# Performance work log

Hardware: AMD Instinct MI355X
Metric: run time of the kernel (lower is better)

The kernel has to match this reference:

```python
import jax, jax.numpy as jnp
import numpy as np

B, N, D = 4, 2048, 256
H, DA, DL = 4, 64, 64          # heads, q/k dim per head, u/v dim per head
NUM_BUCKETS = 128
LN_EPS = 1e-5


def _layernorm(x, g, b):
    mu = jnp.mean(x, axis=-1, keepdims=True)
    var = jnp.var(x, axis=-1, keepdims=True)
    return (x - mu) * jax.lax.rsqrt(var + LN_EPS) * g + b


def setup_inputs() -> dict:
    key = jax.random.key(0)
    ks = jax.random.split(key, 8)
    x = jax.random.normal(ks[0], (B, N, D), jnp.float32)
    lengths = jax.random.randint(ks[1], (B,), 1, N + 1).astype(jnp.int64)
    timestamps = jnp.sort(
        jax.random.randint(ks[2], (B, N), 0, 10_000_000), axis=1
    ).astype(jnp.int64)
    F_uvqk = H * (2 * DL + 2 * DA)
    W_uvqk = jax.random.normal(ks[3], (D, F_uvqk), jnp.float32) * 0.02
    b_uvqk = jnp.zeros((F_uvqk,), jnp.float32)
    W_o = jax.random.normal(ks[4], (H * DL, D), jnp.float32) * 0.02
    b_o = jnp.zeros((D,), jnp.float32)
    ln_in_g = jnp.ones((D,), jnp.float32)
    ln_in_b = jnp.zeros((D,), jnp.float32)
    ln_attn_g = jnp.ones((H * DL,), jnp.float32)
    ln_attn_b = jnp.zeros((H * DL,), jnp.float32)
    w_pos = jax.random.normal(ks[5], (2 * N - 1,), jnp.float32) * 0.02
    w_ts = jax.random.normal(ks[6], (NUM_BUCKETS + 1,), jnp.float32) * 0.02
    return dict(x=x, W_uvqk=W_uvqk, b_uvqk=b_uvqk, W_o=W_o, b_o=b_o,
                ln_in_g=ln_in_g, ln_in_b=ln_in_b,
                ln_attn_g=ln_attn_g, ln_attn_b=ln_attn_b,
                w_pos=w_pos, w_ts=w_ts,
                lengths=lengths, timestamps=timestamps)


def reference(x, W_uvqk, b_uvqk, W_o, b_o, ln_in_g, ln_in_b,
              ln_attn_g, ln_attn_b, w_pos, w_ts, lengths, timestamps):
    # HSTU jagged transduction unit (padded + mask representation).
    nx = _layernorm(x, ln_in_g, ln_in_b)                       # [B,N,D]
    uvqk = jax.nn.silu(nx @ W_uvqk + b_uvqk)                   # fused projection
    u, v, q, k = jnp.split(
        uvqk, [H * DL, 2 * H * DL, 2 * H * DL + H * DA], axis=-1)
    q = q.reshape(B, N, H, DA)
    k = k.reshape(B, N, H, DA)
    v = v.reshape(B, N, H, DL)
    qk = jnp.einsum('bnhd,bmhd->bhnm', q, k)                   # [B,H,N,N]

    # relative position + bucketed relative timestamp bias -> [B,N,N]
    pos = jnp.arange(N)
    pos_bias = w_pos[pos[:, None] - pos[None, :] + (N - 1)]    # [N,N]
    diff = timestamps[:, :, None] - timestamps[:, None, :]     # [B,N,N] int
    bucket = jnp.clip(
        (jnp.log(jnp.maximum(jnp.abs(diff).astype(jnp.float32), 1.0)) / 0.301)
        .astype(jnp.int32), 0, NUM_BUCKETS)
    bias = pos_bias[None] + w_ts[bucket]                       # [B,N,N]

    # non-softmax HSTU attention: silu(scores)/N, causal + valid-key mask
    attn = jax.nn.silu(qk + bias[:, None, :, :]) * (1.0 / N)
    causal = pos[:, None] >= pos[None, :]                      # [N,N]
    valid = pos[None, :] < lengths[:, None]                    # [B,N]
    mask = causal[None, None, :, :] & valid[:, None, None, :]
    attn = jnp.where(mask, attn, 0.0)

    av = jnp.einsum('bhnm,bmhd->bnhd', attn, v).reshape(B, N, H * DL)
    out = (_layernorm(av, ln_attn_g, ln_attn_b) * u) @ W_o + b_o + x
    out = jnp.where(valid[:, :, None], out, 0.0)               # zero padded rows
    return out
```

## Files before the change

kernel.cpp:

```cpp
#include <hip/hip_runtime.h>
#include <stdint.h>

#define BB 4
#define NN 2048
#define DD 256
#define HH 4

typedef __attribute__((ext_vector_type(8))) __bf16 bf16x8;
typedef __attribute__((ext_vector_type(4))) float f32x4;
typedef __attribute__((ext_vector_type(8))) unsigned short u16x8;
typedef __attribute__((ext_vector_type(4))) unsigned short u16x4;

__device__ __forceinline__ unsigned short f2bf(float f) {
  union { float f; uint32_t u; } v; v.f = f;
  uint32_t r = v.u + 0x7fffu + ((v.u >> 16) & 1u);
  return (unsigned short)(r >> 16);
}
__device__ __forceinline__ bf16x8 ld8(const unsigned short* p) {
  return __builtin_bit_cast(bf16x8, *(const u16x8*)p);
}
__device__ __forceinline__ f32x4 mfma16(bf16x8 a, bf16x8 b, f32x4 c) {
  return __builtin_amdgcn_mfma_f32_16x16x32_bf16(a, b, c, 0, 0, 0);
}
__device__ __forceinline__ float silu_f(float x) {
  return x / (1.0f + __expf(-x));
}

__global__ __launch_bounds__(256) void k_prep_w(const float* __restrict__ Wu,
                                                const float* __restrict__ Wo,
                                                unsigned short* __restrict__ Wu_t,
                                                unsigned short* __restrict__ Wo_t) {
  __shared__ float T[64][65];
  int bi = blockIdx.x;
  const float* src; unsigned short* dst; int F, f0, d0;
  if (bi < 64) { src = Wu; dst = Wu_t; F = 1024; f0 = (bi >> 2) * 64; d0 = (bi & 3) * 64; }
  else { int j = bi - 64; src = Wo; dst = Wo_t; F = 256; f0 = (j >> 2) * 64; d0 = (j & 3) * 64; }
  int t = threadIdx.x;
  int li = t >> 4;
  int lj = (t & 15) * 4;
  #pragma unroll
  for (int it = 0; it < 4; ++it) {
    int d = li + it * 16;
    float4 v = *(const float4*)(src + (size_t)(d0 + d) * F + f0 + lj);
    T[lj + 0][d] = v.x; T[lj + 1][d] = v.y; T[lj + 2][d] = v.z; T[lj + 3][d] = v.w;
  }
  __syncthreads();
  #pragma unroll
  for (int it = 0; it < 4; ++it) {
    int f = li + it * 16;
    u16x4 o;
    o[0] = f2bf(T[f][lj + 0]); o[1] = f2bf(T[f][lj + 1]);
    o[2] = f2bf(T[f][lj + 2]); o[3] = f2bf(T[f][lj + 3]);
    *(u16x4*)(dst + (size_t)(f0 + f) * 256 + d0 + lj) = o;
  }
}

__global__ __launch_bounds__(256) void k_ln_in(const float* __restrict__ x,
                                               const float* __restrict__ g,
                                               const float* __restrict__ be,
                                               unsigned short* __restrict__ nx) {
  int wave = threadIdx.x >> 6, lane = threadIdx.x & 63;
  int row = blockIdx.x * 4 + wave;
  const float4 v = *(const float4*)(x + (size_t)row * DD + lane * 4);
  float s = v.x + v.y + v.z + v.w;
  float sq = v.x * v.x + v.y * v.y + v.z * v.z + v.w * v.w;
  #pragma unroll
  for (int o = 32; o; o >>= 1) { s += __shfl_xor(s, o); sq += __shfl_xor(sq, o); }
  float mean = s * (1.0f / DD);
  float var = sq * (1.0f / DD) - mean * mean;
  float rstd = rsqrtf(var + 1e-5f);
  const float4 gv = *(const float4*)(g + lane * 4);
  const float4 bv = *(const float4*)(be + lane * 4);
  u16x4 o4;
  o4[0] = f2bf((v.x - mean) * rstd * gv.x + bv.x);
  o4[1] = f2bf((v.y - mean) * rstd * gv.y + bv.y);
  o4[2] = f2bf((v.z - mean) * rstd * gv.z + bv.z);
  o4[3] = f2bf((v.w - mean) * rstd * gv.w + bv.w);
  *(u16x4*)(nx + (size_t)row * DD + lane * 4) = o4;
}

__global__ __launch_bounds__(256) void k_gemm_uvqk(const unsigned short* __restrict__ nx,
                                                   const unsigned short* __restrict__ Wu_t,
                                                   const float* __restrict__ b_uvqk,
                                                   float* __restrict__ u,
                                                   unsigned short* __restrict__ v_tmp,
                                                   unsigned short* __restrict__ q_t,
                                                   unsigned short* __restrict__ k_t) {
  __shared__ unsigned short As[128 * 72];
  __shared__ unsigned short Bs[128 * 72];
  int tid = threadIdx.x, lane = tid & 63, w = tid >> 6;
  int wr = w >> 1, wc = w & 1, c = lane & 15, g = lane >> 4;
  int rblk = blockIdx.x >> 3, cblk = blockIdx.x & 7;
  int R0 = rblk * 128, C0 = cblk * 128;
  f32x4 acc[4][4] = {};
  for (int ks = 0; ks < 4; ++ks) {
    __syncthreads();
    #pragma unroll
    for (int it = 0; it < 4; ++it) {
      int task = tid + it * 256, row = task >> 3, ch = task & 7;
      *(u16x8*)(As + row * 72 + ch * 8) =
          *(const u16x8*)(nx + (size_t)(R0 + row) * 256 + ks * 64 + ch * 8);
      *(u16x8*)(Bs + row * 72 + ch * 8) =
          *(const u16x8*)(Wu_t + (size_t)(C0 + row) * 256 + ks * 64 + ch * 8);
    }
    __syncthreads();
    #pragma unroll
    for (int kk = 0; kk < 2; ++kk) {
      int koff = kk * 32 + g * 8;
      bf16x8 af[4], bfr[4];
      #pragma unroll
      for (int rt = 0; rt < 4; ++rt) af[rt] = ld8(As + (wr * 64 + rt * 16 + c) * 72 + koff);
      #pragma unroll
      for (int ct = 0; ct < 4; ++ct) bfr[ct] = ld8(Bs + (wc * 64 + ct * 16 + c) * 72 + koff);
      #pragma unroll
      for (int rt = 0; rt < 4; ++rt)
        #pragma unroll
        for (int ct = 0; ct < 4; ++ct)
          acc[rt][ct] = mfma16(af[rt], bfr[ct], acc[rt][ct]);
    }
  }
  #pragma unroll
  for (int rt = 0; rt < 4; ++rt) {
    #pragma unroll
    for (int ct = 0; ct < 4; ++ct) {
      int F = C0 + wc * 64 + ct * 16 + c;
      float bb = b_uvqk[F];
      #pragma unroll
      for (int rr = 0; rr < 4; ++rr) {
        int R = R0 + wr * 64 + rt * 16 + g * 4 + rr;
        float pre = acc[rt][ct][rr] + bb;
        float sv = silu_f(pre);
        int b = R >> 11, n = R & 2047;
        if (F < 256) {
          u[(size_t)R * 256 + F] = sv;
        } else if (F < 512) {
          v_tmp[(size_t)R * 256 + (F - 256)] = f2bf(sv);
        } else if (F < 768) {
          int h = (F - 512) >> 6, d = (F - 512) & 63;
          q_t[((size_t)((b << 2) + h) * 2048 + n) * 64 + d] = f2bf(sv);
        } else {
          int h = (F - 768) >> 6, d = (F - 768) & 63;
          k_t[((size_t)((b << 2) + h) * 2048 + n) * 64 + d] = f2bf(sv);
        }
      }
    }
  }
}

__global__ __launch_bounds__(256) void k_vtrans(const unsigned short* __restrict__ v_tmp,
                                                unsigned short* __restrict__ v_t) {
  __shared__ unsigned short T[64 * 72];
  int bi = blockIdx.x;
  int nch = bi & 31, h = (bi >> 5) & 3, b = bi >> 7;
  int n0 = nch * 64;
  int tid = threadIdx.x;
  #pragma unroll
  for (int it = 0; it < 2; ++it) {
    int task = tid + it * 256;
    int i = task >> 3, ch = task & 7;
    *(u16x8*)(T + i * 72 + ch * 8) =
        *(const u16x8*)(v_tmp + ((size_t)(b * 2048 + n0 + i)) * 256 + h * 64 + ch * 8);
  }
  __syncthreads();
  #pragma unroll
  for (int it = 0; it < 2; ++it) {
    int task = tid + it * 256;
    int d = task >> 3, ch = task & 7;
    u16x8 ov;
    #pragma unroll
    for (int uu = 0; uu < 8; ++uu) ov[uu] = T[(ch * 8 + uu) * 72 + d];
    *(u16x8*)(v_t + ((size_t)((b * 4 + h) * 64 + d)) * 2048 + n0 + ch * 8) = ov;
  }
}

__global__ __launch_bounds__(256) void k_attn(const unsigned short* __restrict__ q_t,
                                              const unsigned short* __restrict__ k_t,
                                              const unsigned short* __restrict__ v_t,
                                              const int* __restrict__ ts_raw,
                                              const int* __restrict__ lens_raw,
                                              const float* __restrict__ w_pos,
                                              const float* __restrict__ w_ts,
                                              float* __restrict__ avP0,
                                              float* __restrict__ avP1) {
  __shared__ unsigned short P_s[4][16 * 72];
  int tid = threadIdx.x, lane = tid & 63, h = tid >> 6;
  int c = lane & 15, g = lane >> 4;
  int bi = blockIdx.x;
  int b, qt, chunk;
  if (bi < 512) { chunk = 0; b = bi & 3; qt = 127 - (bi >> 2); }
  else { chunk = 1; int j = bi - 512; b = j & 3; qt = 127 - (j >> 2); }
  int n0 = qt * 16;
  int stride = (lens_raw[1] == 0 && lens_raw[3] == 0) ? 2 : 1;
  int Lb = lens_raw[b * stride];
  const int* tsb = ts_raw + (size_t)b * 2048 * stride;
  const unsigned short* qp = q_t + (size_t)(b * 4 + h) * 2048 * 64;
  const unsigned short* kp = k_t + (size_t)(b * 4 + h) * 2048 * 64;
  const unsigned short* vp = v_t + (size_t)(b * 4 + h) * 64 * 2048;

  int m_end = min(n0 + 16, Lb);
  int kv_lo = chunk ? 1024 : 0;
  int kv_hi = chunk ? m_end : min(m_end, 1024);

  bf16x8 qf0 = ld8(qp + (size_t)(n0 + c) * 64 + g * 8);
  bf16x8 qf1 = ld8(qp + (size_t)(n0 + c) * 64 + 32 + g * 8);
  int tn[4];
  #pragma unroll
  for (int rr = 0; rr < 4; ++rr) tn[rr] = tsb[(n0 + g * 4 + rr) * stride];
  unsigned short* Pw = &P_s[h][0];
  f32x4 av[4] = {};

  for (int m0 = kv_lo; m0 < kv_hi; m0 += 64) {
    f32x4 s[4] = {};
    #pragma unroll
    for (int mt = 0; mt < 4; ++mt) {
      const unsigned short* kr = kp + (size_t)(m0 + mt * 16 + c) * 64 + g * 8;
      s[mt] = mfma16(qf0, ld8(kr), s[mt]);
      s[mt] = mfma16(qf1, ld8(kr + 32), s[mt]);
    }
    #pragma unroll
    for (int mt = 0; mt < 4; ++mt) {
      int m = m0 + mt * 16 + c;
      int tm = tsb[m * stride];
      #pragma unroll
      for (int rr = 0; rr < 4; ++rr) {
        int n = n0 + g * 4 + rr;
        int dtv = tn[rr] - tm;
        float ad = fmaxf(fabsf((float)dtv), 1.0f);
        int bk = (int)(__log2f(ad) * 2.3028145f);
        bk = bk > 128 ? 128 : bk;
        float sv = s[mt][rr] + w_pos[n - m + 2047] + w_ts[bk];
        float p = (m <= n && m < Lb) ? silu_f(sv) * (1.0f / 2048.0f) : 0.0f;
        Pw[(g * 4 + rr) * 72 + mt * 16 + c] = f2bf(p);
      }
    }
    #pragma unroll
    for (int kk = 0; kk < 2; ++kk) {
      bf16x8 pa = ld8(Pw + c * 72 + kk * 32 + g * 8);
      #pragma unroll
      for (int dt = 0; dt < 4; ++dt) {
        bf16x8 vf = ld8(vp + (size_t)(dt * 16 + c) * 2048 + m0 + kk * 32 + g * 8);
        av[dt] = mfma16(pa, vf, av[dt]);
      }
    }
  }

  if (chunk == 0) {
    #pragma unroll
    for (int dt = 0; dt < 4; ++dt)
      #pragma unroll
      for (int rr = 0; rr < 4; ++rr) {
        int n = n0 + g * 4 + rr;
        avP0[((size_t)(b * 2048 + n)) * 256 + h * 64 + dt * 16 + c] = av[dt][rr];
      }
  } else {
    #pragma unroll
    for (int dt = 0; dt < 4; ++dt)
      #pragma unroll
      for (int rr = 0; rr < 4; ++rr) {
        int n = n0 + g * 4 + rr;
        avP1[((size_t)(b * 1024 + (n - 1024))) * 256 + h * 64 + dt * 16 + c] = av[dt][rr];
      }
  }
}

__global__ __launch_bounds__(256) void k_ln_attn(const float* __restrict__ avP0,
                                                 const float* __restrict__ avP1,
                                                 const float* __restrict__ u,
                                                 const float* __restrict__ g,
                                                 const float* __restrict__ be,
                                                 unsigned short* __restrict__ a2) {
  int wave = threadIdx.x >> 6, lane = threadIdx.x & 63;
  int row = blockIdx.x * 4 + wave;
  int n = row & 2047, b = row >> 11;
  float4 v = *(const float4*)(avP0 + (size_t)row * DD + lane * 4);
  if (n >= 1024) {
    const float4 w = *(const float4*)(avP1 + ((size_t)(b * 1024 + (n - 1024))) * DD + lane * 4);
    v.x += w.x; v.y += w.y; v.z += w.z; v.w += w.w;
  }
  float s = v.x + v.y + v.z + v.w;
  float sq = v.x * v.x + v.y * v.y + v.z * v.z + v.w * v.w;
  #pragma unroll
  for (int o = 32; o; o >>= 1) { s += __shfl_xor(s, o); sq += __shfl_xor(sq, o); }
  float mean = s * (1.0f / DD);
  float var = sq * (1.0f / DD) - mean * mean;
  float rstd = rsqrtf(var + 1e-5f);
  const float4 gv = *(const float4*)(g + lane * 4);
  const float4 bv = *(const float4*)(be + lane * 4);
  const float4 uv = *(const float4*)(u + (size_t)row * DD + lane * 4);
  u16x4 o4;
  o4[0] = f2bf(((v.x - mean) * rstd * gv.x + bv.x) * uv.x);
  o4[1] = f2bf(((v.y - mean) * rstd * gv.y + bv.y) * uv.y);
  o4[2] = f2bf(((v.z - mean) * rstd * gv.z + bv.z) * uv.z);
  o4[3] = f2bf(((v.w - mean) * rstd * gv.w + bv.w) * uv.w);
  *(u16x4*)(a2 + (size_t)row * DD + lane * 4) = o4;
}

__global__ __launch_bounds__(256) void k_gemm_out(const unsigned short* __restrict__ a2,
                                                  const unsigned short* __restrict__ Wo_t,
                                                  const float* __restrict__ b_o,
                                                  const float* __restrict__ x,
                                                  const int* __restrict__ lens_raw,
                                                  float* __restrict__ out) {
  __shared__ unsigned short As[64 * 72];
  __shared__ unsigned short Bs[64 * 72];
  int tid = threadIdx.x, lane = tid & 63, w = tid >> 6;
  int wr = w >> 1, wc = w & 1, c = lane & 15, g = lane >> 4;
  int rblk = blockIdx.x >> 2, cblk = blockIdx.x & 3;
  int R0 = rblk * 64, C0 = cblk * 64;
  int stride = (lens_raw[1] == 0 && lens_raw[3] == 0) ? 2 : 1;
  f32x4 acc[2][2] = {};
  for (int ks = 0; ks < 4; ++ks) {
    __syncthreads();
    #pragma unroll
    for (int it = 0; it < 2; ++it) {
      int task = tid + it * 256, row = task >> 3, ch = task & 7;
      *(u16x8*)(As + row * 72 + ch * 8) =
          *(const u16x8*)(a2 + (size_t)(R0 + row) * 256 + ks * 64 + ch * 8);
      *(u16x8*)(Bs + row * 72 + ch * 8) =
          *(const u16x8*)(Wo_t + (size_t)(C0 + row) * 256 + ks * 64 + ch * 8);
    }
    __syncthreads();
    #pragma unroll
    for (int kk = 0; kk < 2; ++kk) {
      int koff = kk * 32 + g * 8;
      bf16x8 af[2], bfr[2];
      #pragma unroll
      for (int rt = 0; rt < 2; ++rt) af[rt] = ld8(As + (wr * 32 + rt * 16 + c) * 72 + koff);
      #pragma unroll
      for (int ct = 0; ct < 2; ++ct) bfr[ct] = ld8(Bs + (wc * 32 + ct * 16 + c) * 72 + koff);
      #pragma unroll
      for (int rt = 0; rt < 2; ++rt)
        #pragma unroll
        for (int ct = 0; ct < 2; ++ct)
          acc[rt][ct] = mfma16(af[rt], bfr[ct], acc[rt][ct]);
    }
  }
  #pragma unroll
  for (int rt = 0; rt < 2; ++rt) {
    #pragma unroll
    for (int ct = 0; ct < 2; ++ct) {
      int F = C0 + wc * 32 + ct * 16 + c;
      float bo = b_o[F];
      #pragma unroll
      for (int rr = 0; rr < 4; ++rr) {
        int R = R0 + wr * 32 + rt * 16 + g * 4 + rr;
        int b = R >> 11, n = R & 2047;
        int Lb = lens_raw[b * stride];
        float val = acc[rt][ct][rr] + bo + x[(size_t)R * 256 + F];
        out[(size_t)R * 256 + F] = (n < Lb) ? val : 0.0f;
      }
    }
  }
}

extern "C" void kernel_launch(void* const* d_in, const int* in_sizes, int n_in,
                              void* d_out, int out_size, void* d_ws, size_t ws_size,
                              hipStream_t stream) {
  const float* x        = (const float*)d_in[0];
  const float* W_uvqk   = (const float*)d_in[1];
  const float* b_uvqk   = (const float*)d_in[2];
  const float* W_o      = (const float*)d_in[3];
  const float* b_o      = (const float*)d_in[4];
  const float* ln_in_g  = (const float*)d_in[5];
  const float* ln_in_b  = (const float*)d_in[6];
  const float* ln_attn_g= (const float*)d_in[7];
  const float* ln_attn_b= (const float*)d_in[8];
  const float* w_pos    = (const float*)d_in[9];
  const float* w_ts     = (const float*)d_in[10];
  const int*   lengths  = (const int*)d_in[11];
  const int*   tstamps  = (const int*)d_in[12];
  float* out = (float*)d_out;

  char* ws = (char*)d_ws;
  size_t off = 0;
  auto alloc = [&](size_t bytes) -> void* {
    void* p = ws + off;
    off += (bytes + 255) & ~(size_t)255;
    return p;
  };
  unsigned short* Wu_t  = (unsigned short*)alloc(1024 * 256 * 2);
  unsigned short* Wo_t  = (unsigned short*)alloc(256 * 256 * 2);
  unsigned short* nx    = (unsigned short*)alloc((size_t)8192 * 256 * 2);
  float*          u     = (float*)alloc((size_t)8192 * 256 * 4);
  unsigned short* v_tmp = (unsigned short*)alloc((size_t)8192 * 256 * 2);
  unsigned short* v_t   = (unsigned short*)alloc((size_t)8192 * 256 * 2);
  unsigned short* q_t   = (unsigned short*)alloc((size_t)8192 * 256 * 2);
  unsigned short* k_t   = (unsigned short*)alloc((size_t)8192 * 256 * 2);
  float*          avP0  = (float*)alloc((size_t)8192 * 256 * 4);
  unsigned short* a2    = (unsigned short*)alloc((size_t)8192 * 256 * 2);
  float*          avP1  = (float*)nx;

  k_prep_w<<<80, 256, 0, stream>>>(W_uvqk, W_o, Wu_t, Wo_t);
  k_ln_in<<<2048, 256, 0, stream>>>(x, ln_in_g, ln_in_b, nx);
  k_gemm_uvqk<<<512, 256, 0, stream>>>(nx, Wu_t, b_uvqk, u, v_tmp, q_t, k_t);
  k_vtrans<<<512, 256, 0, stream>>>(v_tmp, v_t);
  k_attn<<<768, 256, 0, stream>>>(q_t, k_t, v_t, tstamps, lengths, w_pos, w_ts, avP0, avP1);
  k_ln_attn<<<2048, 256, 0, stream>>>(avP0, avP1, u, ln_attn_g, ln_attn_b, a2);
  k_gemm_out<<<512, 256, 0, stream>>>(a2, Wo_t, b_o, x, lengths, out);
}
```

Before: 237.1 us.

## Precompute position and timestamp bias once per batch, shared across heads

Adds a k_bias kernel that computes the bucketed timestamp bias plus the relative-position bias once per batch, only for causal and valid tiles, and stores it as bf16 in a packed triangular tile layout. The attention kernel then loads this bias instead of recomputing the log, bucket and two gathers for every head. This removes redundant transcendental and gather work that was repeated four times, once per head. In exchange it adds an extra kernel launch, a bias buffer of roughly 17 MB (aliased with v_tmp and extended), and bf16 rounding of the bias values.

```diff
diff --git a/kernel.cpp b/kernel.cpp
--- a/kernel.cpp
+++ b/kernel.cpp
@@ -16,6 +16,9 @@
   uint32_t r = v.u + 0x7fffu + ((v.u >> 16) & 1u);
   return (unsigned short)(r >> 16);
 }
+__device__ __forceinline__ float bf2f(unsigned short u) {
+  union { uint32_t u; float f; } v; v.u = ((uint32_t)u) << 16; return v.f;
+}
 __device__ __forceinline__ bf16x8 ld8(const unsigned short* p) {
   return __builtin_bit_cast(bf16x8, *(const u16x8*)p);
 }
@@ -24,6 +27,10 @@
 }
 __device__ __forceinline__ float silu_f(float x) {
   return x / (1.0f + __expf(-x));
+}
+__device__ __forceinline__ int bias_off(int qt) {
+  int a = qt >> 2, r = qt & 3;
+  return (a + 1) * (2 * a + r);
 }
 
 __global__ __launch_bounds__(256) void k_prep_w(const float* __restrict__ Wu,
@@ -173,13 +180,42 @@
   }
 }
 
+__global__ __launch_bounds__(256) void k_bias(const int* __restrict__ ts_raw,
+                                              const int* __restrict__ lens_raw,
+                                              const float* __restrict__ w_pos,
+                                              const float* __restrict__ w_ts,
+                                              unsigned short* __restrict__ bias_t) {
+  int bi = blockIdx.x;
+  int b = bi >> 12, qt = (bi >> 5) & 127, mc = bi & 31;
+  if (mc > (qt >> 2)) return;
+  int stride = (lens_raw[1] == 0 && lens_raw[3] == 0) ? 2 : 1;
+  int Lb = lens_raw[b * stride];
+  if (mc * 64 >= Lb) return;
+  const int* tsb = ts_raw + (size_t)b * 2048 * stride;
+  int t = threadIdx.x;
+  int l = t >> 2, mt = t & 3;
+  int m = mc * 64 + mt * 16 + (l & 15);
+  int nbase = qt * 16 + ((l >> 4) << 2);
+  int tm = tsb[m * stride];
+  size_t tile = (size_t)(b * 2112 + bias_off(qt) + mc);
+  u16x4 o;
+  #pragma unroll
+  for (int j = 0; j < 4; ++j) {
+    int n = nbase + j;
+    int dtv = tsb[n * stride] - tm;
+    float ad = fmaxf(fabsf((float)dtv), 1.0f);
+    int bk = (int)(__log2f(ad) * 2.3028145f);
+    bk = bk > 128 ? 128 : bk;
+    o[j] = f2bf(w_pos[n - m + 2047] + w_ts[bk]);
+  }
+  *(u16x4*)(bias_t + tile * 1024 + t * 4) = o;
+}
+
 __global__ __launch_bounds__(256) void k_attn(const unsigned short* __restrict__ q_t,
                                               const unsigned short* __restrict__ k_t,
                                               const unsigned short* __restrict__ v_t,
-                                              const int* __restrict__ ts_raw,
+                                              const unsigned short* __restrict__ bias_t,
                                               const int* __restrict__ lens_raw,
-                                              const float* __restrict__ w_pos,
-                                              const float* __restrict__ w_ts,
                                               float* __restrict__ avP0,
                                               float* __restrict__ avP1) {
   __shared__ unsigned short P_s[4][16 * 72];
@@ -192,10 +228,10 @@
   int n0 = qt * 16;
   int stride = (lens_raw[1] == 0 && lens_raw[3] == 0) ? 2 : 1;
   int Lb = lens_raw[b * stride];
-  const int* tsb = ts_raw + (size_t)b * 2048 * stride;
   const unsigned short* qp = q_t + (size_t)(b * 4 + h) * 2048 * 64;
   const unsigned short* kp = k_t + (size_t)(b * 4 + h) * 2048 * 64;
   const unsigned short* vp = v_t + (size_t)(b * 4 + h) * 64 * 2048;
+  const unsigned short* btile = bias_t + ((size_t)(b * 2112 + bias_off(qt))) * 1024 + lane * 16;
 
   int m_end = min(n0 + 16, Lb);
   int kv_lo = chunk ? 1024 : 0;
@@ -203,13 +239,13 @@
 
   bf16x8 qf0 = ld8(qp + (size_t)(n0 + c) * 64 + g * 8);
   bf16x8 qf1 = ld8(qp + (size_t)(n0 + c) * 64 + 32 + g * 8);
-  int tn[4];
-  #pragma unroll
-  for (int rr = 0; rr < 4; ++rr) tn[rr] = tsb[(n0 + g * 4 + rr) * stride];
   unsigned short* Pw = &P_s[h][0];
   f32x4 av[4] = {};
 
   for (int m0 = kv_lo; m0 < kv_hi; m0 += 64) {
+    const unsigned short* bp = btile + (size_t)(m0 >> 6) * 1024;
+    u16x8 bt0 = *(const u16x8*)bp;
+    u16x8 bt1 = *(const u16x8*)(bp + 8);
     f32x4 s[4] = {};
     #pragma unroll
     for (int mt = 0; mt < 4; ++mt) {
@@ -220,15 +256,12 @@
     #pragma unroll
     for (int mt = 0; mt < 4; ++mt) {
       int m = m0 + mt * 16 + c;
-      int tm = tsb[m * stride];
       #pragma unroll
       for (int rr = 0; rr < 4; ++rr) {
         int n = n0 + g * 4 + rr;
-        int dtv = tn[rr] - tm;
-        float ad = fmaxf(fabsf((float)dtv), 1.0f);
-        int bk = (int)(__log2f(ad) * 2.3028145f);
-        bk = bk > 128 ? 128 : bk;
-        float sv = s[mt][rr] + w_pos[n - m + 2047] + w_ts[bk];
+        int idx = mt * 4 + rr;
+        unsigned short ub = idx < 8 ? bt0[idx] : bt1[idx - 8];
+        float sv = s[mt][rr] + bf2f(ub);
         float p = (m <= n && m < Lb) ? silu_f(sv) * (1.0f / 2048.0f) : 0.0f;
         Pw[(g * 4 + rr) * 72 + mt * 16 + c] = f2bf(p);
       }
@@ -382,19 +415,22 @@
   unsigned short* Wo_t  = (unsigned short*)alloc(256 * 256 * 2);
   unsigned short* nx    = (unsigned short*)alloc((size_t)8192 * 256 * 2);
   float*          u     = (float*)alloc((size_t)8192 * 256 * 4);
-  unsigned short* v_tmp = (unsigned short*)alloc((size_t)8192 * 256 * 2);
   unsigned short* v_t   = (unsigned short*)alloc((size_t)8192 * 256 * 2);
   unsigned short* q_t   = (unsigned short*)alloc((size_t)8192 * 256 * 2);
   unsigned short* k_t   = (unsigned short*)alloc((size_t)8192 * 256 * 2);
   float*          avP0  = (float*)alloc((size_t)8192 * 256 * 4);
   unsigned short* a2    = (unsigned short*)alloc((size_t)8192 * 256 * 2);
+  unsigned short* v_tmp = (unsigned short*)alloc((size_t)8192 * 256 * 2);
+  unsigned short* bias_t = (unsigned short*)v_tmp;
+  (void)alloc((size_t)4 * 2112 * 1024 * 2 - (size_t)8192 * 256 * 2);
   float*          avP1  = (float*)nx;
 
   k_prep_w<<<80, 256, 0, stream>>>(W_uvqk, W_o, Wu_t, Wo_t);
   k_ln_in<<<2048, 256, 0, stream>>>(x, ln_in_g, ln_in_b, nx);
   k_gemm_uvqk<<<512, 256, 0, stream>>>(nx, Wu_t, b_uvqk, u, v_tmp, q_t, k_t);
   k_vtrans<<<512, 256, 0, stream>>>(v_tmp, v_t);
-  k_attn<<<768, 256, 0, stream>>>(q_t, k_t, v_t, tstamps, lengths, w_pos, w_ts, avP0, avP1);
+  k_bias<<<16384, 256, 0, stream>>>(tstamps, lengths, w_pos, w_ts, bias_t);
+  k_attn<<<768, 256, 0, stream>>>(q_t, k_t, v_t, bias_t, lengths, avP0, avP1);
   k_ln_attn<<<2048, 256, 0, stream>>>(avP0, avP1, u, ln_attn_g, ln_attn_b, a2);
   k_gemm_out<<<512, 256, 0, stream>>>(a2, Wo_t, b_o, x, lengths, out);
 }
```

After: 221.5 us. 6.6% less time.
